# Performance work log

Hardware: AMD Instinct MI355X
Metric: run time of the kernel (lower is better)

## Reference

```python
import jax, jax.numpy as jnp
import numpy as np
import math

D_MODEL = 1024
N_HEADS = 16
D_K = D_MODEL // N_HEADS


def setup_inputs() -> dict:
    key = jax.random.key(0)
    ks = jax.random.split(key, 9)
    B, N = 2, 8192
    s = 1.0 / math.sqrt(D_MODEL)
    x = jax.random.normal(ks[0], (B, N, D_MODEL), dtype=jnp.float32)
    Wq = jax.random.normal(ks[1], (D_MODEL, D_MODEL), dtype=jnp.float32) * s
    bq = jnp.zeros((D_MODEL,), dtype=jnp.float32)
    Wk = jax.random.normal(ks[2], (D_MODEL, D_MODEL), dtype=jnp.float32) * s
    bk = jnp.zeros((D_MODEL,), dtype=jnp.float32)
    Wv = jax.random.normal(ks[3], (D_MODEL, D_MODEL), dtype=jnp.float32) * s
    bv = jnp.zeros((D_MODEL,), dtype=jnp.float32)
    Wo = jax.random.normal(ks[4], (D_MODEL, D_MODEL), dtype=jnp.float32) * s
    bo = jnp.zeros((D_MODEL,), dtype=jnp.float32)
    return {"x": x, "Wq": Wq, "bq": bq, "Wk": Wk, "bk": bk,
            "Wv": Wv, "bv": bv, "Wo": Wo, "bo": bo}


def _fft_circulant_attention(Q, K, V):
    # Q,K,V: (B,H,N,d_k); FFT along the sequence axis (axis=2)
    B, H, N, d_k = Q.shape
    scale = 1.0 / math.sqrt(d_k)
    Q_fft = jnp.fft.rfft(Q, axis=2)
    K_fft = jnp.fft.rfft(K, axis=2)
    # circular cross-correlation summed over d_k -> (B,H,Nf)
    scores_fft = jnp.sum(Q_fft * jnp.conj(K_fft), axis=-1)
    scores = jnp.fft.irfft(scores_fft, n=N, axis=2) * scale  # (B,H,N)
    attn = jax.nn.softmax(scores, axis=-1)                    # (B,H,N)
    attn_fft = jnp.fft.rfft(attn, axis=2)                     # (B,H,Nf)
    V_fft = jnp.fft.rfft(V, axis=2)                           # (B,H,Nf,d_k)
    out_fft = attn_fft[..., None] * V_fft
    return jnp.fft.irfft(out_fft, n=N, axis=2)                # (B,H,N,d_k)


def reference(x, Wq, bq, Wk, bk, Wv, bv, Wo, bo):
    B, N, _ = x.shape
    # torch Linear: x @ W.T + b
    def proj(W, b):
        return (x @ W.T + b).reshape(B, N, N_HEADS, D_K).transpose(0, 2, 1, 3)
    Q = proj(Wq, bq)
    K = proj(Wk, bk)
    V = proj(Wv, bv)
    O = _fft_circulant_attention(Q, K, V)          # (B,H,N,d_k)
    O = O.transpose(0, 2, 1, 3).reshape(B, N, D_MODEL)
    return O @ Wo.T + bo
```

## Files before the change

### kernel.cpp

```cpp
#include <hip/hip_runtime.h>
#include <math.h>
#include <stdint.h>

#define NDIM 8192
#define DM 1024
#define NH 16
#define DKH 64
#define BATCH 2
#define NSPLIT 16
#define NT 512
#define NPT (NDIM / NT)

typedef __attribute__((ext_vector_type(8))) short short8v;
typedef __attribute__((ext_vector_type(4))) float f32x4;

__device__ inline float bf2f(unsigned short u) {
  return __uint_as_float(((unsigned int)u) << 16);
}
__device__ inline unsigned short f2bf(float f) {
  unsigned int u = __float_as_uint(f);
  u += 0x7fffu + ((u >> 16) & 1u);
  return (unsigned short)(u >> 16);
}
__device__ inline float2 cmul(float2 a, float2 b) {
  return make_float2(a.x * b.x - a.y * b.y, a.x * b.y + a.y * b.x);
}
__device__ inline float2 cmulc(float2 a, float2 b) {
  return make_float2(a.x * b.x + a.y * b.y, a.y * b.x - a.x * b.y);
}

__device__ inline void gload_lds16(const void* g, void* l) {
  __builtin_amdgcn_global_load_lds(
      (const __attribute__((address_space(1))) unsigned int*)(uintptr_t)g,
      (__attribute__((address_space(3))) unsigned int*)(uintptr_t)l, 16, 0, 0);
}

__global__ void twiddle_init(float2* tw) {
  int k = blockIdx.x * blockDim.x + threadIdx.x;
  if (k < NDIM) {
    double a = -2.0 * 3.14159265358979323846 * (double)k / (double)NDIM;
    tw[k] = make_float2((float)cos(a), (float)sin(a));
  }
}

__global__ __launch_bounds__(256)
void split_x(const float* __restrict__ x, unsigned short* __restrict__ xhi,
             unsigned short* __restrict__ xlo) {
  size_t i = ((size_t)blockIdx.x * 256 + threadIdx.x) * 4;
  float4 v = *(const float4*)&x[i];
  ushort4 h, l;
  h.x = f2bf(v.x); l.x = f2bf(v.x - bf2f(h.x));
  h.y = f2bf(v.y); l.y = f2bf(v.y - bf2f(h.y));
  h.z = f2bf(v.z); l.z = f2bf(v.z - bf2f(h.z));
  h.w = f2bf(v.w); l.w = f2bf(v.w - bf2f(h.w));
  *(ushort4*)&xhi[i] = h;
  *(ushort4*)&xlo[i] = l;
}

__global__ __launch_bounds__(256)
void split_w(const float* __restrict__ Wq, const float* __restrict__ Wk,
             const float* __restrict__ Wv, const float* __restrict__ Wo,
             unsigned short* __restrict__ whi, unsigned short* __restrict__ wlo,
             unsigned short* __restrict__ wob) {
  int z = blockIdx.z;
  const float* W = (z == 0) ? Wq : ((z == 1) ? Wk : ((z == 2) ? Wv : Wo));
  size_t i = ((size_t)blockIdx.x * 256 + threadIdx.x) * 4;
  float4 v = *(const float4*)&W[i];
  ushort4 h, l;
  h.x = f2bf(v.x); l.x = f2bf(v.x - bf2f(h.x));
  h.y = f2bf(v.y); l.y = f2bf(v.y - bf2f(h.y));
  h.z = f2bf(v.z); l.z = f2bf(v.z - bf2f(h.z));
  h.w = f2bf(v.w); l.w = f2bf(v.w - bf2f(h.w));
  if (z < 3) {
    *(ushort4*)&whi[(size_t)z * DM * DM + i] = h;
    *(ushort4*)&wlo[(size_t)z * DM * DM + i] = l;
  } else {
    *(ushort4*)&wob[i] = h;
  }
}

__device__ inline void fft_fwd(float2* __restrict__ s, const float2* __restrict__ tw, int tid) {
  const float C = 0.70710678118654752f;
  for (int lm = 10; lm >= 1; lm -= 3) {
    int m = 1 << lm;
    int sh = 10 - lm;
    __syncthreads();
    for (int t = tid; t < NDIM / 8; t += NT) {
      int p = t & (m - 1);
      int i0 = ((t >> lm) << (lm + 3)) + p;
      float2 x0 = s[i0],       x1 = s[i0 + m],     x2 = s[i0 + 2 * m], x3 = s[i0 + 3 * m];
      float2 x4 = s[i0 + 4 * m], x5 = s[i0 + 5 * m], x6 = s[i0 + 6 * m], x7 = s[i0 + 7 * m];
      float2 e0 = {x0.x + x4.x, x0.y + x4.y}, o0 = {x0.x - x4.x, x0.y - x4.y};
      float2 e1 = {x1.x + x5.x, x1.y + x5.y}, o1 = {x1.x - x5.x, x1.y - x5.y};
      float2 e2 = {x2.x + x6.x, x2.y + x6.y}, o2 = {x2.x - x6.x, x2.y - x6.y};
      float2 e3 = {x3.x + x7.x, x3.y + x7.y}, o3 = {x3.x - x7.x, x3.y - x7.y};
      float2 t1 = {C * (o1.x + o1.y), C * (o1.y - o1.x)};
      float2 t2 = {o2.y, -o2.x};
      float2 t3 = {C * (o3.y - o3.x), -C * (o3.x + o3.y)};
      float2 pe = {e0.x + e2.x, e0.y + e2.y}, qe = {e0.x - e2.x, e0.y - e2.y};
      float2 re = {e1.x + e3.x, e1.y + e3.y}, se = {e1.x - e3.x, e1.y - e3.y};
      float2 po = {o0.x + t2.x, o0.y + t2.y}, qo = {o0.x - t2.x, o0.y - t2.y};
      float2 ro = {t1.x + t3.x, t1.y + t3.y}, so = {t1.x - t3.x, t1.y - t3.y};
      float2 y0 = {pe.x + re.x, pe.y + re.y};
      float2 y4 = {pe.x - re.x, pe.y - re.y};
      float2 y2 = {qe.x + se.y, qe.y - se.x};
      float2 y6 = {qe.x - se.y, qe.y + se.x};
      float2 y1 = {po.x + ro.x, po.y + ro.y};
      float2 y5 = {po.x - ro.x, po.y - ro.y};
      float2 y3 = {qo.x + so.y, qo.y - so.x};
      float2 y7 = {qo.x - so.y, qo.y + so.x};
      int e = p << sh;
      s[i0]         = y0;
      s[i0 + m]     = cmul(y1, tw[e]);
      s[i0 + 2 * m] = cmul(y2, tw[2 * e]);
      s[i0 + 3 * m] = cmul(y3, tw[3 * e]);
      s[i0 + 4 * m] = cmul(y4, tw[4 * e]);
      s[i0 + 5 * m] = cmul(y5, tw[5 * e]);
      s[i0 + 6 * m] = cmul(y6, tw[6 * e]);
      s[i0 + 7 * m] = cmul(y7, tw[7 * e]);
    }
  }
  __syncthreads();
  for (int t = tid; t < NDIM / 2; t += NT) {
    int i0 = t * 2;
    float2 u = s[i0], v = s[i0 + 1];
    s[i0]     = make_float2(u.x + v.x, u.y + v.y);
    s[i0 + 1] = make_float2(u.x - v.x, u.y - v.y);
  }
  __syncthreads();
}

__device__ inline void fft_inv(float2* __restrict__ s, const float2* __restrict__ tw, int tid) {
  const float C = 0.70710678118654752f;
  __syncthreads();
  for (int t = tid; t < NDIM / 2; t += NT) {
    int i0 = t * 2;
    float2 u = s[i0], v = s[i0 + 1];
    s[i0]     = make_float2(u.x + v.x, u.y + v.y);
    s[i0 + 1] = make_float2(u.x - v.x, u.y - v.y);
  }
  for (int lm = 1; lm <= 10; lm += 3) {
    int m = 1 << lm;
    int sh = 10 - lm;
    __syncthreads();
    for (int t = tid; t < NDIM / 8; t += NT) {
      int p = t & (m - 1);
      int i0 = ((t >> lm) << (lm + 3)) + p;
      int e = p << sh;
      float2 z0 = s[i0];
      float2 z1 = cmulc(s[i0 + m],     tw[e]);
      float2 z2 = cmulc(s[i0 + 2 * m], tw[2 * e]);
      float2 z3 = cmulc(s[i0 + 3 * m], tw[3 * e]);
      float2 z4 = cmulc(s[i0 + 4 * m], tw[4 * e]);
      float2 z5 = cmulc(s[i0 + 5 * m], tw[5 * e]);
      float2 z6 = cmulc(s[i0 + 6 * m], tw[6 * e]);
      float2 z7 = cmulc(s[i0 + 7 * m], tw[7 * e]);
      float2 E0 = {z0.x + z4.x, z0.y + z4.y}, O0 = {z0.x - z4.x, z0.y - z4.y};
      float2 E1 = {z1.x + z5.x, z1.y + z5.y}, O1 = {z1.x - z5.x, z1.y - z5.y};
      float2 E2 = {z2.x + z6.x, z2.y + z6.y}, O2 = {z2.x - z6.x, z2.y - z6.y};
      float2 E3 = {z3.x + z7.x, z3.y + z7.y}, O3 = {z3.x - z7.x, z3.y - z7.y};
      float2 T1 = {C * (O1.x - O1.y), C * (O1.x + O1.y)};
      float2 T2 = {-O2.y, O2.x};
      float2 T3 = {-C * (O3.x + O3.y), C * (O3.x - O3.y)};
      float2 PE = {E0.x + E2.x, E0.y + E2.y}, QE = {E0.x - E2.x, E0.y - E2.y};
      float2 RE = {E1.x + E3.x, E1.y + E3.y}, SE = {E1.x - E3.x, E1.y - E3.y};
      float2 PO = {O0.x + T2.x, O0.y + T2.y}, QO = {O0.x - T2.x, O0.y - T2.y};
      float2 RO = {T1.x + T3.x, T1.y + T3.y}, SO = {T1.x - T3.x, T1.y - T3.y};
      s[i0]         = make_float2(PE.x + RE.x, PE.y + RE.y);
      s[i0 + 4 * m] = make_float2(PE.x - RE.x, PE.y - RE.y);
      s[i0 + 2 * m] = make_float2(QE.x - SE.y, QE.y + SE.x);
      s[i0 + 6 * m] = make_float2(QE.x + SE.y, QE.y - SE.x);
      s[i0 + m]     = make_float2(PO.x + RO.x, PO.y + RO.y);
      s[i0 + 5 * m] = make_float2(PO.x - RO.x, PO.y - RO.y);
      s[i0 + 3 * m] = make_float2(QO.x - SO.y, QO.y + SO.x);
      s[i0 + 7 * m] = make_float2(QO.x + SO.y, QO.y - SO.x);
    }
  }
  __syncthreads();
}

__device__ inline float blk_max(float v, float* red, int tid) {
  #pragma unroll
  for (int o = 32; o > 0; o >>= 1) v = fmaxf(v, __shfl_down(v, o, 64));
  __syncthreads();
  if ((tid & 63) == 0) red[tid >> 6] = v;
  __syncthreads();
  float r = fmaxf(fmaxf(fmaxf(red[0], red[1]), fmaxf(red[2], red[3])),
                  fmaxf(fmaxf(red[4], red[5]), fmaxf(red[6], red[7])));
  __syncthreads();
  return r;
}
__device__ inline float blk_sum(float v, float* red, int tid) {
  #pragma unroll
  for (int o = 32; o > 0; o >>= 1) v += __shfl_down(v, o, 64);
  __syncthreads();
  if ((tid & 63) == 0) red[tid >> 6] = v;
  __syncthreads();
  float r = ((red[0] + red[1]) + (red[2] + red[3])) + ((red[4] + red[5]) + (red[6] + red[7]));
  __syncthreads();
  return r;
}

__global__ __launch_bounds__(512, 4)
void proj_gemm_mfma(const unsigned short* __restrict__ xhi, const unsigned short* __restrict__ xlo,
                    const unsigned short* __restrict__ whi, const unsigned short* __restrict__ wlo,
                    const float* __restrict__ bq, const float* __restrict__ bk,
                    const float* __restrict__ bv,
                    float* __restrict__ Qt, float* __restrict__ Kt, unsigned short* __restrict__ Vt) {
  int z = blockIdx.z;
  int b = z / 3, wsel = z % 3;
  bool full = (wsel < 2);
  const unsigned short* Wh = whi + (size_t)wsel * DM * DM;
  const unsigned short* Wl = wlo + (size_t)wsel * DM * DM;
  const float* bias = (wsel == 0) ? bq : ((wsel == 1) ? bk : bv);
  int cb = blockIdx.y * 128;
  int nb = blockIdx.x * 128;
  __shared__ unsigned short lAh[128 * 64], lAl[128 * 64];
  __shared__ unsigned short lBh[128 * 64], lBl[128 * 64];
  int tid = threadIdx.x;
  int lane = tid & 63, wid = tid >> 6;
  int wr = wid >> 2, wc = wid & 3;
  int srow = tid >> 3, sg = tid & 7;
  const unsigned short* gAh = Wh + (size_t)cb * DM;
  const unsigned short* gAl = Wl + (size_t)cb * DM;
  const unsigned short* gBh = xhi + ((size_t)b * NDIM + nb) * DM;
  const unsigned short* gBl = xlo + ((size_t)b * NDIM + nb) * DM;

  f32x4 acc[4][2];
  #pragma unroll
  for (int i = 0; i < 4; ++i)
    #pragma unroll
    for (int j = 0; j < 2; ++j) acc[i][j] = (f32x4){0.f, 0.f, 0.f, 0.f};

  int col = lane & 15, kg = lane >> 4;
  for (int k0 = 0; k0 < DM; k0 += 64) {
    #pragma unroll
    for (int i = 0; i < 2; ++i) {
      int r = i * 64 + srow;
      int gc = (sg ^ (r & 7)) * 8;
      size_t go = (size_t)r * DM + k0 + gc;
      int lo_ = r * 64 + sg * 8;
      gload_lds16(gAh + go, &lAh[lo_]);
      gload_lds16(gBh + go, &lBh[lo_]);
      if (full) {
        gload_lds16(gAl + go, &lAl[lo_]);
        gload_lds16(gBl + go, &lBl[lo_]);
      }
    }
    asm volatile("s_waitcnt vmcnt(0)");
    __syncthreads();
    #pragma unroll
    for (int kk = 0; kk < 2; ++kk) {
      short8v ah[4], al[4], bh_[2], bl_[2];
      #pragma unroll
      for (int mi = 0; mi < 4; ++mi) {
        int r = wr * 64 + mi * 16 + col;
        int s = r * 64 + (((kk * 4 + kg) ^ (r & 7)) * 8);
        ah[mi] = *(const short8v*)&lAh[s];
        if (full) al[mi] = *(const short8v*)&lAl[s];
      }
      #pragma unroll
      for (int ni = 0; ni < 2; ++ni) {
        int r = wc * 32 + ni * 16 + col;
        int s = r * 64 + (((kk * 4 + kg) ^ (r & 7)) * 8);
        bh_[ni] = *(const short8v*)&lBh[s];
        if (full) bl_[ni] = *(const short8v*)&lBl[s];
      }
      #pragma unroll
      for (int mi = 0; mi < 4; ++mi)
        #pragma unroll
        for (int ni = 0; ni < 2; ++ni) {
          acc[mi][ni] = __builtin_amdgcn_mfma_f32_16x16x32_bf16(ah[mi], bh_[ni], acc[mi][ni], 0, 0, 0);
          if (full) {
            acc[mi][ni] = __builtin_amdgcn_mfma_f32_16x16x32_bf16(ah[mi], bl_[ni], acc[mi][ni], 0, 0, 0);
            acc[mi][ni] = __builtin_amdgcn_mfma_f32_16x16x32_bf16(al[mi], bh_[ni], acc[mi][ni], 0, 0, 0);
          }
        }
    }
    __syncthreads();
  }
  size_t obase = (size_t)b * DM * NDIM;
  #pragma unroll
  for (int mi = 0; mi < 4; ++mi) {
    #pragma unroll
    for (int reg = 0; reg < 4; ++reg) {
      int c = cb + wr * 64 + mi * 16 + kg * 4 + reg;
      float bsv = bias[c];
      #pragma unroll
      for (int ni = 0; ni < 2; ++ni) {
        int n = nb + wc * 32 + ni * 16 + col;
        float v = acc[mi][ni][reg] + bsv;
        if (wsel < 2) {
          float* out = ((wsel == 0) ? Qt : Kt) + obase;
          out[(size_t)c * NDIM + n] = v;
        } else {
          Vt[obase + (size_t)c * NDIM + n] = f2bf(v);
        }
      }
    }
  }
}

__global__ __launch_bounds__(512, 4)
void score_fft_kernel(const float* __restrict__ Qt, const float* __restrict__ Kt,
                      const float2* __restrict__ tw, float2* __restrict__ part) {
  extern __shared__ float2 buf[];
  int bh = blockIdx.x / NSPLIT;
  int split = blockIdx.x % NSPLIT;
  int b = bh / NH, h = bh % NH;
  int tid = threadIdx.x;
  float qfx[NPT], qfy[NPT], accx[NPT], accy[NPT];
  #pragma unroll
  for (int i = 0; i < NPT; ++i) { accx[i] = 0.f; accy[i] = 0.f; }

  for (int dp = 0; dp < 2; ++dp) {
    int c0 = h * DKH + (split * 2 + dp) * 2;
    const float* q0 = Qt + ((size_t)b * DM + c0) * NDIM;
    const float* q1 = q0 + NDIM;
    const float* k0c = Kt + ((size_t)b * DM + c0) * NDIM;
    const float* k1c = k0c + NDIM;
    #pragma unroll
    for (int i = 0; i < NPT; ++i) {
      int ii = i * NT + tid;
      buf[ii] = make_float2(q0[ii], q1[ii]);
    }
    fft_fwd(buf, tw, tid);
    #pragma unroll
    for (int i = 0; i < NPT; ++i) { float2 v = buf[i * NT + tid]; qfx[i] = v.x; qfy[i] = v.y; }
    #pragma unroll
    for (int i = 0; i < NPT; ++i) {
      int ii = i * NT + tid;
      buf[ii] = make_float2(k0c[ii], k1c[ii]);
    }
    fft_fwd(buf, tw, tid);
    #pragma unroll
    for (int i = 0; i < NPT; ++i) {
      float2 kf = buf[i * NT + tid];
      accx[i] += qfx[i] * kf.x + qfy[i] * kf.y;
      accy[i] += qfy[i] * kf.x - qfx[i] * kf.y;
    }
  }
  float2* dst = part + ((size_t)bh * NSPLIT + split) * NDIM;
  #pragma unroll
  for (int i = 0; i < NPT; ++i) dst[i * NT + tid] = make_float2(accx[i], accy[i]);
}

__global__ __launch_bounds__(256)
void reduce_part(const float2* __restrict__ part, float2* __restrict__ sred) {
  #pragma unroll
  for (int rep = 0; rep < 2; ++rep) {
    size_t g = (size_t)blockIdx.x * 512 + rep * 256 + threadIdx.x;
    int bh = (int)(g >> 13);
    int i  = (int)(g & (NDIM - 1));
    float sx = 0.f, sy = 0.f;
    #pragma unroll
    for (int s = 0; s < NSPLIT; ++s) {
      float2 v = part[((size_t)bh * NSPLIT + s) * NDIM + i];
      sx += v.x; sy += v.y;
    }
    sred[g] = make_float2(sx, sy);
  }
}

__global__ __launch_bounds__(512, 4)
void softmax_attn_kernel(const float2* __restrict__ sred, const float2* __restrict__ tw,
                         float2* __restrict__ attnf) {
  extern __shared__ float2 buf[];
  int bh = blockIdx.x;
  int tid = threadIdx.x;
  for (int i = tid; i < NDIM; i += NT) buf[i] = sred[(size_t)bh * NDIM + i];
  fft_inv(buf, tw, tid);
  const float scale = 0.125f / (float)NDIM;
  float vals[NPT];
  float lmax = -3.0e38f;
  #pragma unroll
  for (int i = 0; i < NPT; ++i) {
    float v = buf[i * NT + tid].x * scale;
    vals[i] = v;
    lmax = fmaxf(lmax, v);
  }
  float* red = (float*)buf;
  float gmax = blk_max(lmax, red, tid);
  float lsum = 0.f;
  #pragma unroll
  for (int i = 0; i < NPT; ++i) { float e = expf(vals[i] - gmax); vals[i] = e; lsum += e; }
  float gsum = blk_sum(lsum, red, tid);
  float inv = 1.0f / gsum;
  #pragma unroll
  for (int i = 0; i < NPT; ++i) buf[i * NT + tid] = make_float2(vals[i] * inv, 0.f);
  fft_fwd(buf, tw, tid);
  for (int i = tid; i < NDIM; i += NT) attnf[(size_t)bh * NDIM + i] = buf[i];
}

__global__ __launch_bounds__(512, 4)
void out_fft_kernel(const unsigned short* __restrict__ Vt, const float2* __restrict__ attnf,
                    const float2* __restrict__ tw, unsigned short* __restrict__ Ot) {
  extern __shared__ float2 buf[];
  int idx = blockIdx.x;
  int b = idx / (DM / 2), cp = idx % (DM / 2);
  int c0 = cp * 2;
  int h = c0 >> 6;
  int bh = b * NH + h;
  int tid = threadIdx.x;
  const unsigned short* v0 = Vt + ((size_t)b * DM + c0) * NDIM;
  const unsigned short* v1 = v0 + NDIM;
  for (int i = tid; i < NDIM; i += NT) buf[i] = make_float2(bf2f(v0[i]), bf2f(v1[i]));
  fft_fwd(buf, tw, tid);
  for (int i = tid; i < NDIM; i += NT) {
    float2 vf = buf[i];
    float2 af = attnf[(size_t)bh * NDIM + i];
    buf[i] = cmul(vf, af);
  }
  fft_inv(buf, tw, tid);
  const float invn = 1.0f / (float)NDIM;
  unsigned short* o0 = Ot + ((size_t)b * DM + c0) * NDIM;
  unsigned short* o1 = o0 + NDIM;
  for (int i = tid; i < NDIM; i += NT) {
    float2 v = buf[i];
    o0[i] = f2bf(v.x * invn);
    o1[i] = f2bf(v.y * invn);
  }
}

__global__ __launch_bounds__(256)
void transpose_ot(const unsigned short* __restrict__ Ot, unsigned short* __restrict__ Ont) {
  int b = blockIdx.z;
  int cb = blockIdx.y * 64, n0 = blockIdx.x * 64;
  __shared__ unsigned short t[64][68];
  int tid = threadIdx.x;
  int r = tid >> 4, c4 = (tid & 15) * 4;
  const unsigned short* src = Ot + (size_t)b * DM * NDIM;
  #pragma unroll
  for (int i = 0; i < 4; ++i) {
    ushort4 v = *(const ushort4*)&src[(size_t)(cb + i * 16 + r) * NDIM + n0 + c4];
    *(ushort4*)&t[i * 16 + r][c4] = v;
  }
  __syncthreads();
  unsigned short* dst = Ont + (size_t)b * NDIM * DM;
  #pragma unroll
  for (int i = 0; i < 4; ++i) {
    int n = i * 16 + r;
    ushort4 v;
    v.x = t[c4 + 0][n]; v.y = t[c4 + 1][n]; v.z = t[c4 + 2][n]; v.w = t[c4 + 3][n];
    *(ushort4*)&dst[(size_t)(n0 + n) * DM + cb + c4] = v;
  }
}

__global__ __launch_bounds__(512, 4)
void final_gemm_mfma(const unsigned short* __restrict__ Ont, const unsigned short* __restrict__ Wob,
                     const float* __restrict__ bo, float* __restrict__ out) {
  int b = blockIdx.z;
  int nb = blockIdx.x * 128;
  int pb = blockIdx.y * 128;
  __shared__ unsigned short lA[128 * 64], lB[128 * 64];
  int tid = threadIdx.x;
  int lane = tid & 63, wid = tid >> 6;
  int wr = wid >> 2, wc = wid & 3;
  int srow = tid >> 3, sg = tid & 7;
  const unsigned short* gA = Ont + ((size_t)b * NDIM + nb) * DM;
  const unsigned short* gB = Wob + (size_t)pb * DM;

  f32x4 acc[4][2];
  #pragma unroll
  for (int i = 0; i < 4; ++i)
    #pragma unroll
    for (int j = 0; j < 2; ++j) acc[i][j] = (f32x4){0.f, 0.f, 0.f, 0.f};

  int col = lane & 15, kg = lane >> 4;
  for (int k0 = 0; k0 < DM; k0 += 64) {
    #pragma unroll
    for (int i = 0; i < 2; ++i) {
      int r = i * 64 + srow;
      int gc = (sg ^ (r & 7)) * 8;
      size_t go = (size_t)r * DM + k0 + gc;
      int lo_ = r * 64 + sg * 8;
      gload_lds16(gA + go, &lA[lo_]);
      gload_lds16(gB + go, &lB[lo_]);
    }
    asm volatile("s_waitcnt vmcnt(0)");
    __syncthreads();
    #pragma unroll
    for (int kk = 0; kk < 2; ++kk) {
      short8v af[4], bf[2];
      #pragma unroll
      for (int mi = 0; mi < 4; ++mi) {
        int r = wr * 64 + mi * 16 + col;
        af[mi] = *(const short8v*)&lA[r * 64 + (((kk * 4 + kg) ^ (r & 7)) * 8)];
      }
      #pragma unroll
      for (int ni = 0; ni < 2; ++ni) {
        int r = wc * 32 + ni * 16 + col;
        bf[ni] = *(const short8v*)&lB[r * 64 + (((kk * 4 + kg) ^ (r & 7)) * 8)];
      }
      #pragma unroll
      for (int mi = 0; mi < 4; ++mi)
        #pragma unroll
        for (int ni = 0; ni < 2; ++ni)
          acc[mi][ni] = __builtin_amdgcn_mfma_f32_16x16x32_bf16(af[mi], bf[ni], acc[mi][ni], 0, 0, 0);
    }
    __syncthreads();
  }
  #pragma unroll
  for (int mi = 0; mi < 4; ++mi) {
    #pragma unroll
    for (int reg = 0; reg < 4; ++reg) {
      int n = nb + wr * 64 + mi * 16 + kg * 4 + reg;
      size_t rowoff = ((size_t)b * NDIM + n) * DM;
      #pragma unroll
      for (int ni = 0; ni < 2; ++ni) {
        int cp = pb + wc * 32 + ni * 16 + col;
        out[rowoff + cp] = acc[mi][ni][reg] + bo[cp];
      }
    }
  }
}

extern "C" void kernel_launch(void* const* d_in, const int* in_sizes, int n_in,
                              void* d_out, int out_size, void* d_ws, size_t ws_size,
                              hipStream_t stream) {
  (void)in_sizes; (void)n_in; (void)out_size;
  const float* x  = (const float*)d_in[0];
  const float* Wq = (const float*)d_in[1]; const float* bq = (const float*)d_in[2];
  const float* Wk = (const float*)d_in[3]; const float* bk = (const float*)d_in[4];
  const float* Wv = (const float*)d_in[5]; const float* bv = (const float*)d_in[6];
  const float* Wo = (const float*)d_in[7]; const float* bo = (const float*)d_in[8];

  char* ws = (char*)d_ws;
  size_t off = 0;
  float2* tw = (float2*)(ws + off); off += (size_t)NDIM * sizeof(float2);
  float*  Qt = (float*)(ws + off);  off += (size_t)BATCH * DM * NDIM * 4;
  float*  Kt = (float*)(ws + off);  off += (size_t)BATCH * DM * NDIM * 4;
  unsigned short* Vt  = (unsigned short*)(ws + off); off += (size_t)BATCH * DM * NDIM * 2;
  size_t xhi_off = off;
  unsigned short* Xhi = (unsigned short*)(ws + off); off += (size_t)BATCH * NDIM * DM * 2;
  size_t xlo_off = off;
  unsigned short* Xlo = (unsigned short*)(ws + off); off += (size_t)BATCH * NDIM * DM * 2;
  unsigned short* Whi = (unsigned short*)(ws + off); off += (size_t)3 * DM * DM * 2;
  unsigned short* Wlo = (unsigned short*)(ws + off); off += (size_t)3 * DM * DM * 2;
  unsigned short* Wob = (unsigned short*)(ws + off); off += (size_t)DM * DM * 2;
  float2* part  = (float2*)(ws + xhi_off);
  float2* attnf = (float2*)(ws + xlo_off);
  float2* sred  = (float2*)(ws + xlo_off + 4194304);
  unsigned short* Ot  = (unsigned short*)Qt;
  unsigned short* Ont = (unsigned short*)Kt;

  if (ws_size < off) return;

  twiddle_init<<<32, 256, 0, stream>>>(tw);
  split_x<<<(BATCH * NDIM * DM) / (256 * 4), 256, 0, stream>>>(x, Xhi, Xlo);
  split_w<<<dim3((DM * DM) / (256 * 4), 1, 4), 256, 0, stream>>>(Wq, Wk, Wv, Wo, Whi, Wlo, Wob);

  dim3 pg(NDIM / 128, DM / 128, 3 * BATCH);
  proj_gemm_mfma<<<pg, 512, 0, stream>>>(Xhi, Xlo, Whi, Wlo, bq, bk, bv, Qt, Kt, Vt);

  score_fft_kernel<<<BATCH * NH * NSPLIT, NT, NDIM * sizeof(float2), stream>>>(Qt, Kt, tw, part);
  reduce_part<<<(BATCH * NH * NDIM) / 512, 256, 0, stream>>>(part, sred);
  softmax_attn_kernel<<<BATCH * NH, NT, NDIM * sizeof(float2), stream>>>(sred, tw, attnf);
  out_fft_kernel<<<BATCH * DM / 2, NT, NDIM * sizeof(float2), stream>>>(Vt, attnf, tw, Ot);

  transpose_ot<<<dim3(NDIM / 64, DM / 64, BATCH), 256, 0, stream>>>(Ot, Ont);
  final_gemm_mfma<<<dim3(NDIM / 128, DM / 128, BATCH), 512, 0, stream>>>(Ont, Wob, bo, (float*)d_out);
}
```

Before: 523.0 us.

## Double-buffer GEMM LDS tiles and shrink FFT kernel blocks to 256 threads

Both MFMA GEMM kernels now keep two shared-memory stages, issuing the next k-tile's global-to-LDS loads before computing on the current one, so load latency can overlap compute. This doubles LDS per block (128KB for the projection, 64KB for the final GEMM) and lowers the occupancy hint to 2. Separately, the FFT, score and softmax kernels drop from 512 to 256 threads per block, which doubles per-thread register arrays and work per thread. The block reductions are cut to four wavefronts to match. Note that the proj loop no longer has an explicit vmcnt wait before reading the staged buffer, which risks reading LDS before the async loads land.

```diff
diff --git a/kernel.cpp b/kernel.cpp
--- a/kernel.cpp
+++ b/kernel.cpp
@@ -8,8 +8,8 @@
 #define DKH 64
 #define BATCH 2
 #define NSPLIT 16
-#define NT 512
-#define NPT (NDIM / NT)
+#define NTF 256
+#define NPTF (NDIM / NTF)
 
 typedef __attribute__((ext_vector_type(8))) short short8v;
 typedef __attribute__((ext_vector_type(4))) float f32x4;
@@ -85,7 +85,7 @@
     int m = 1 << lm;
     int sh = 10 - lm;
     __syncthreads();
-    for (int t = tid; t < NDIM / 8; t += NT) {
+    for (int t = tid; t < NDIM / 8; t += NTF) {
       int p = t & (m - 1);
       int i0 = ((t >> lm) << (lm + 3)) + p;
       float2 x0 = s[i0],       x1 = s[i0 + m],     x2 = s[i0 + 2 * m], x3 = s[i0 + 3 * m];
@@ -121,7 +121,7 @@
     }
   }
   __syncthreads();
-  for (int t = tid; t < NDIM / 2; t += NT) {
+  for (int t = tid; t < NDIM / 2; t += NTF) {
     int i0 = t * 2;
     float2 u = s[i0], v = s[i0 + 1];
     s[i0]     = make_float2(u.x + v.x, u.y + v.y);
@@ -133,7 +133,7 @@
 __device__ inline void fft_inv(float2* __restrict__ s, const float2* __restrict__ tw, int tid) {
   const float C = 0.70710678118654752f;
   __syncthreads();
-  for (int t = tid; t < NDIM / 2; t += NT) {
+  for (int t = tid; t < NDIM / 2; t += NTF) {
     int i0 = t * 2;
     float2 u = s[i0], v = s[i0 + 1];
     s[i0]     = make_float2(u.x + v.x, u.y + v.y);
@@ -143,7 +143,7 @@
     int m = 1 << lm;
     int sh = 10 - lm;
     __syncthreads();
-    for (int t = tid; t < NDIM / 8; t += NT) {
+    for (int t = tid; t < NDIM / 8; t += NTF) {
       int p = t & (m - 1);
       int i0 = ((t >> lm) << (lm + 3)) + p;
       int e = p << sh;
@@ -185,8 +185,7 @@
   __syncthreads();
   if ((tid & 63) == 0) red[tid >> 6] = v;
   __syncthreads();
-  float r = fmaxf(fmaxf(fmaxf(red[0], red[1]), fmaxf(red[2], red[3])),
-                  fmaxf(fmaxf(red[4], red[5]), fmaxf(red[6], red[7])));
+  float r = fmaxf(fmaxf(red[0], red[1]), fmaxf(red[2], red[3]));
   __syncthreads();
   return r;
 }
@@ -196,17 +195,18 @@
   __syncthreads();
   if ((tid & 63) == 0) red[tid >> 6] = v;
   __syncthreads();
-  float r = ((red[0] + red[1]) + (red[2] + red[3])) + ((red[4] + red[5]) + (red[6] + red[7]));
+  float r = (red[0] + red[1]) + (red[2] + red[3]);
   __syncthreads();
   return r;
 }
 
-__global__ __launch_bounds__(512, 4)
+__global__ __launch_bounds__(512, 2)
 void proj_gemm_mfma(const unsigned short* __restrict__ xhi, const unsigned short* __restrict__ xlo,
                     const unsigned short* __restrict__ whi, const unsigned short* __restrict__ wlo,
                     const float* __restrict__ bq, const float* __restrict__ bk,
                     const float* __restrict__ bv,
                     float* __restrict__ Qt, float* __restrict__ Kt, unsigned short* __restrict__ Vt) {
+  extern __shared__ unsigned short smem[];
   int z = blockIdx.z;
   int b = z / 3, wsel = z % 3;
   bool full = (wsel < 2);
@@ -215,8 +215,6 @@
   const float* bias = (wsel == 0) ? bq : ((wsel == 1) ? bk : bv);
   int cb = blockIdx.y * 128;
   int nb = blockIdx.x * 128;
-  __shared__ unsigned short lAh[128 * 64], lAl[128 * 64];
-  __shared__ unsigned short lBh[128 * 64], lBl[128 * 64];
   int tid = threadIdx.x;
   int lane = tid & 63, wid = tid >> 6;
   int wr = wid >> 2, wc = wid & 3;
@@ -233,22 +231,33 @@
     for (int j = 0; j < 2; ++j) acc[i][j] = (f32x4){0.f, 0.f, 0.f, 0.f};
 
   int col = lane & 15, kg = lane >> 4;
-  for (int k0 = 0; k0 < DM; k0 += 64) {
+
+  auto stage = [&](int buf, int k0) {
+    unsigned short* base = smem + buf * 32768;
     #pragma unroll
     for (int i = 0; i < 2; ++i) {
       int r = i * 64 + srow;
       int gc = (sg ^ (r & 7)) * 8;
       size_t go = (size_t)r * DM + k0 + gc;
       int lo_ = r * 64 + sg * 8;
-      gload_lds16(gAh + go, &lAh[lo_]);
-      gload_lds16(gBh + go, &lBh[lo_]);
+      gload_lds16(gAh + go, base + lo_);
+      gload_lds16(gBh + go, base + 8192 + lo_);
       if (full) {
-        gload_lds16(gAl + go, &lAl[lo_]);
-        gload_lds16(gBl + go, &lBl[lo_]);
-      }
-    }
-    asm volatile("s_waitcnt vmcnt(0)");
-    __syncthreads();
+        gload_lds16(gAl + go, base + 16384 + lo_);
+        gload_lds16(gBl + go, base + 24576 + lo_);
+      }
+    }
+  };
+
+  stage(0, 0);
+  __syncthreads();
+  int cur = 0;
+  for (int t = 0; t < 16; ++t) {
+    if (t < 15) stage(cur ^ 1, (t + 1) * 64);
+    const unsigned short* pAh = smem + cur * 32768;
+    const unsigned short* pBh = pAh + 8192;
+    const unsigned short* pAl = pAh + 16384;
+    const unsigned short* pBl = pAh + 24576;
     #pragma unroll
     for (int kk = 0; kk < 2; ++kk) {
       short8v ah[4], al[4], bh_[2], bl_[2];
@@ -256,15 +265,15 @@
       for (int mi = 0; mi < 4; ++mi) {
         int r = wr * 64 + mi * 16 + col;
         int s = r * 64 + (((kk * 4 + kg) ^ (r & 7)) * 8);
-        ah[mi] = *(const short8v*)&lAh[s];
-        if (full) al[mi] = *(const short8v*)&lAl[s];
+        ah[mi] = *(const short8v*)&pAh[s];
+        if (full) al[mi] = *(const short8v*)&pAl[s];
       }
       #pragma unroll
       for (int ni = 0; ni < 2; ++ni) {
         int r = wc * 32 + ni * 16 + col;
         int s = r * 64 + (((kk * 4 + kg) ^ (r & 7)) * 8);
-        bh_[ni] = *(const short8v*)&lBh[s];
-        if (full) bl_[ni] = *(const short8v*)&lBl[s];
+        bh_[ni] = *(const short8v*)&pBh[s];
+        if (full) bl_[ni] = *(const short8v*)&pBl[s];
       }
       #pragma unroll
       for (int mi = 0; mi < 4; ++mi)
@@ -278,6 +287,7 @@
         }
     }
     __syncthreads();
+    cur ^= 1;
   }
   size_t obase = (size_t)b * DM * NDIM;
   #pragma unroll
@@ -301,7 +311,7 @@
   }
 }
 
-__global__ __launch_bounds__(512, 4)
+__global__ __launch_bounds__(256)
 void score_fft_kernel(const float* __restrict__ Qt, const float* __restrict__ Kt,
                       const float2* __restrict__ tw, float2* __restrict__ part) {
   extern __shared__ float2 buf[];
@@ -309,9 +319,9 @@
   int split = blockIdx.x % NSPLIT;
   int b = bh / NH, h = bh % NH;
   int tid = threadIdx.x;
-  float qfx[NPT], qfy[NPT], accx[NPT], accy[NPT];
-  #pragma unroll
-  for (int i = 0; i < NPT; ++i) { accx[i] = 0.f; accy[i] = 0.f; }
+  float qfx[NPTF], qfy[NPTF], accx[NPTF], accy[NPTF];
+  #pragma unroll
+  for (int i = 0; i < NPTF; ++i) { accx[i] = 0.f; accy[i] = 0.f; }
 
   for (int dp = 0; dp < 2; ++dp) {
     int c0 = h * DKH + (split * 2 + dp) * 2;
@@ -320,29 +330,29 @@
     const float* k0c = Kt + ((size_t)b * DM + c0) * NDIM;
     const float* k1c = k0c + NDIM;
     #pragma unroll
-    for (int i = 0; i < NPT; ++i) {
-      int ii = i * NT + tid;
+    for (int i = 0; i < NPTF; ++i) {
+      int ii = i * NTF + tid;
       buf[ii] = make_float2(q0[ii], q1[ii]);
     }
     fft_fwd(buf, tw, tid);
     #pragma unroll
-    for (int i = 0; i < NPT; ++i) { float2 v = buf[i * NT + tid]; qfx[i] = v.x; qfy[i] = v.y; }
-    #pragma unroll
-    for (int i = 0; i < NPT; ++i) {
-      int ii = i * NT + tid;
+    for (int i = 0; i < NPTF; ++i) { float2 v = buf[i * NTF + tid]; qfx[i] = v.x; qfy[i] = v.y; }
+    #pragma unroll
+    for (int i = 0; i < NPTF; ++i) {
+      int ii = i * NTF + tid;
       buf[ii] = make_float2(k0c[ii], k1c[ii]);
     }
     fft_fwd(buf, tw, tid);
     #pragma unroll
-    for (int i = 0; i < NPT; ++i) {
-      float2 kf = buf[i * NT + tid];
+    for (int i = 0; i < NPTF; ++i) {
+      float2 kf = buf[i * NTF + tid];
       accx[i] += qfx[i] * kf.x + qfy[i] * kf.y;
       accy[i] += qfy[i] * kf.x - qfx[i] * kf.y;
     }
   }
   float2* dst = part + ((size_t)bh * NSPLIT + split) * NDIM;
   #pragma unroll
-  for (int i = 0; i < NPT; ++i) dst[i * NT + tid] = make_float2(accx[i], accy[i]);
+  for (int i = 0; i < NPTF; ++i) dst[i * NTF + tid] = make_float2(accx[i], accy[i]);
 }
 
 __global__ __launch_bounds__(256)
@@ -362,20 +372,20 @@
   }
 }
 
-__global__ __launch_bounds__(512, 4)
+__global__ __launch_bounds__(256)
 void softmax_attn_kernel(const float2* __restrict__ sred, const float2* __restrict__ tw,
                          float2* __restrict__ attnf) {
   extern __shared__ float2 buf[];
   int bh = blockIdx.x;
   int tid = threadIdx.x;
-  for (int i = tid; i < NDIM; i += NT) buf[i] = sred[(size_t)bh * NDIM + i];
+  for (int i = tid; i < NDIM; i += NTF) buf[i] = sred[(size_t)bh * NDIM + i];
   fft_inv(buf, tw, tid);
   const float scale = 0.125f / (float)NDIM;
-  float vals[NPT];
+  float vals[NPTF];
   float lmax = -3.0e38f;
   #pragma unroll
-  for (int i = 0; i < NPT; ++i) {
-    float v = buf[i * NT + tid].x * scale;
+  for (int i = 0; i < NPTF; ++i) {
+    float v = buf[i * NTF + tid].x * scale;
     vals[i] = v;
     lmax = fmaxf(lmax, v);
   }
@@ -383,16 +393,16 @@
   float gmax = blk_max(lmax, red, tid);
   float lsum = 0.f;
   #pragma unroll
-  for (int i = 0; i < NPT; ++i) { float e = expf(vals[i] - gmax); vals[i] = e; lsum += e; }
+  for (int i = 0; i < NPTF; ++i) { float e = expf(vals[i] - gmax); vals[i] = e; lsum += e; }
   float gsum = blk_sum(lsum, red, tid);
   float inv = 1.0f / gsum;
   #pragma unroll
-  for (int i = 0; i < NPT; ++i) buf[i * NT + tid] = make_float2(vals[i] * inv, 0.f);
+  for (int i = 0; i < NPTF; ++i) buf[i * NTF + tid] = make_float2(vals[i] * inv, 0.f);
   fft_fwd(buf, tw, tid);
-  for (int i = tid; i < NDIM; i += NT) attnf[(size_t)bh * NDIM + i] = buf[i];
-}
-
-__global__ __launch_bounds__(512, 4)
+  for (int i = tid; i < NDIM; i += NTF) attnf[(size_t)bh * NDIM + i] = buf[i];
+}
+
+__global__ __launch_bounds__(256)
 void out_fft_kernel(const unsigned short* __restrict__ Vt, const float2* __restrict__ attnf,
                     const float2* __restrict__ tw, unsigned short* __restrict__ Ot) {
   extern __shared__ float2 buf[];
@@ -404,9 +414,9 @@
   int tid = threadIdx.x;
   const unsigned short* v0 = Vt + ((size_t)b * DM + c0) * NDIM;
   const unsigned short* v1 = v0 + NDIM;
-  for (int i = tid; i < NDIM; i += NT) buf[i] = make_float2(bf2f(v0[i]), bf2f(v1[i]));
+  for (int i = tid; i < NDIM; i += NTF) buf[i] = make_float2(bf2f(v0[i]), bf2f(v1[i]));
   fft_fwd(buf, tw, tid);
-  for (int i = tid; i < NDIM; i += NT) {
+  for (int i = tid; i < NDIM; i += NTF) {
     float2 vf = buf[i];
     float2 af = attnf[(size_t)bh * NDIM + i];
     buf[i] = cmul(vf, af);
@@ -415,7 +425,7 @@
   const float invn = 1.0f / (float)NDIM;
   unsigned short* o0 = Ot + ((size_t)b * DM + c0) * NDIM;
   unsigned short* o1 = o0 + NDIM;
-  for (int i = tid; i < NDIM; i += NT) {
+  for (int i = tid; i < NDIM; i += NTF) {
     float2 v = buf[i];
     o0[i] = f2bf(v.x * invn);
     o1[i] = f2bf(v.y * invn);
@@ -446,13 +456,13 @@
   }
 }
 
-__global__ __launch_bounds__(512, 4)
+__global__ __launch_bounds__(512, 2)
 void final_gemm_mfma(const unsigned short* __restrict__ Ont, const unsigned short* __restrict__ Wob,
                      const float* __restrict__ bo, float* __restrict__ out) {
+  extern __shared__ unsigned short smem[];
   int b = blockIdx.z;
   int nb = blockIdx.x * 128;
   int pb = blockIdx.y * 128;
-  __shared__ unsigned short lA[128 * 64], lB[128 * 64];
   int tid = threadIdx.x;
   int lane = tid & 63, wid = tid >> 6;
   int wr = wid >> 2, wc = wid & 3;
@@ -467,30 +477,39 @@
     for (int j = 0; j < 2; ++j) acc[i][j] = (f32x4){0.f, 0.f, 0.f, 0.f};
 
   int col = lane & 15, kg = lane >> 4;
-  for (int k0 = 0; k0 < DM; k0 += 64) {
+
+  auto stage = [&](int buf, int k0) {
+    unsigned short* base = smem + buf * 16384;
     #pragma unroll
     for (int i = 0; i < 2; ++i) {
       int r = i * 64 + srow;
       int gc = (sg ^ (r & 7)) * 8;
       size_t go = (size_t)r * DM + k0 + gc;
       int lo_ = r * 64 + sg * 8;
-      gload_lds16(gA + go, &lA[lo_]);
-      gload_lds16(gB + go, &lB[lo_]);
-    }
-    asm volatile("s_waitcnt vmcnt(0)");
-    __syncthreads();
+      gload_lds16(gA + go, base + lo_);
+      gload_lds16(gB + go, base + 8192 + lo_);
+    }
+  };
+
+  stage(0, 0);
+  __syncthreads();
+  int cur = 0;
+  for (int t = 0; t < 16; ++t) {
+    if (t < 15) stage(cur ^ 1, (t + 1) * 64);
+    const unsigned short* pA = smem + cur * 16384;
+    const unsigned short* pB = pA + 8192;
     #pragma unroll
     for (int kk = 0; kk < 2; ++kk) {
       short8v af[4], bf[2];
       #pragma unroll
       for (int mi = 0; mi < 4; ++mi) {
         int r = wr * 64 + mi * 16 + col;
-        af[mi] = *(const short8v*)&lA[r * 64 + (((kk * 4 + kg) ^ (r & 7)) * 8)];
+        af[mi] = *(const short8v*)&pA[r * 64 + (((kk * 4 + kg) ^ (r & 7)) * 8)];
       }
       #pragma unroll
       for (int ni = 0; ni < 2; ++ni) {
         int r = wc * 32 + ni * 16 + col;
-        bf[ni] = *(const short8v*)&lB[r * 64 + (((kk * 4 + kg) ^ (r & 7)) * 8)];
+        bf[ni] = *(const short8v*)&pB[r * 64 + (((kk * 4 + kg) ^ (r & 7)) * 8)];
       }
       #pragma unroll
       for (int mi = 0; mi < 4; ++mi)
@@ -499,6 +518,7 @@
           acc[mi][ni] = __builtin_amdgcn_mfma_f32_16x16x32_bf16(af[mi], bf[ni], acc[mi][ni], 0, 0, 0);
     }
     __syncthreads();
+    cur ^= 1;
   }
   #pragma unroll
   for (int mi = 0; mi < 4; ++mi) {
@@ -551,13 +571,13 @@
   split_w<<<dim3((DM * DM) / (256 * 4), 1, 4), 256, 0, stream>>>(Wq, Wk, Wv, Wo, Whi, Wlo, Wob);
 
   dim3 pg(NDIM / 128, DM / 128, 3 * BATCH);
-  proj_gemm_mfma<<<pg, 512, 0, stream>>>(Xhi, Xlo, Whi, Wlo, bq, bk, bv, Qt, Kt, Vt);
-
-  score_fft_kernel<<<BATCH * NH * NSPLIT, NT, NDIM * sizeof(float2), stream>>>(Qt, Kt, tw, part);
+  proj_gemm_mfma<<<pg, 512, 131072, stream>>>(Xhi, Xlo, Whi, Wlo, bq, bk, bv, Qt, Kt, Vt);
+
+  score_fft_kernel<<<BATCH * NH * NSPLIT, NTF, NDIM * sizeof(float2), stream>>>(Qt, Kt, tw, part);
   reduce_part<<<(BATCH * NH * NDIM) / 512, 256, 0, stream>>>(part, sred);
-  softmax_attn_kernel<<<BATCH * NH, NT, NDIM * sizeof(float2), stream>>>(sred, tw, attnf);
-  out_fft_kernel<<<BATCH * DM / 2, NT, NDIM * sizeof(float2), stream>>>(Vt, attnf, tw, Ot);
+  softmax_attn_kernel<<<BATCH * NH, NTF, NDIM * sizeof(float2), stream>>>(sred, tw, attnf);
+  out_fft_kernel<<<BATCH * DM / 2, NTF, NDIM * sizeof(float2), stream>>>(Vt, attnf, tw, Ot);
 
   transpose_ot<<<dim3(NDIM / 64, DM / 64, BATCH), 256, 0, stream>>>(Ot, Ont);
-  final_gemm_mfma<<<dim3(NDIM / 128, DM / 128, BATCH), 512, 0, stream>>>(Ont, Wob, bo, (float*)d_out);
-}
+  final_gemm_mfma<<<dim3(NDIM / 128, DM / 128, BATCH), 512, 65536, stream>>>(Ont, Wob, bo, (float*)d_out);
+}
```

Measured after the change: 543.3 us. 1.04x slower.
